# Kernel tuning notes

Measured on AMD Instinct MI355X. Metric: run time of the kernel, lower is better.

## Reference

```python
import jax, jax.numpy as jnp
import numpy as np

# --- constants from cfg (dmc.__init__) ---
DT = 3600.0            # self.t
P_SPATIAL = 21.0       # cfg.params.defaults.p
VEL_LB, VEL_UB = 0.3, 15.0
DEPTH_LB = 0.01
Q_LB = 1e-4            # discharge lower bound
BW_LB = 0.1            # bottom width lower bound
SLOPE_MIN = 1e-4
N_LO, N_HI = 0.01, 0.35          # Manning n bounds (denormalize)
QS_LO, QS_HI = 0.0, 3.0          # q_spatial bounds

# --- river network: perfect binary confluence tree, topologically ordered ---
LEVELS = 17
SIZES = [2 ** (LEVELS - 1 - l) for l in range(LEVELS)]   # 65536 leaves ... 1 outlet
OFFS = np.concatenate([[0], np.cumsum(SIZES)]).astype(np.int64)
N_NODES = int(OFFS[-1])  # 131071; internal nodes are indices OFFS[1]..N_NODES-1 (contiguous)


def _tree_edges():
    src, dst, cl, cr = [], [], [], []
    for l in range(1, LEVELS):
        k = np.arange(SIZES[l], dtype=np.int64)
        p = OFFS[l] + k
        c0 = OFFS[l - 1] + 2 * k
        c1 = OFFS[l - 1] + 2 * k + 1
        src += [c0, c1]
        dst += [p, p]
        cl.append(c0)
        cr.append(c1)
    return (np.concatenate(src).astype(np.int32), np.concatenate(dst).astype(np.int32),
            np.concatenate(cl).astype(np.int32), np.concatenate(cr).astype(np.int32))


def setup_inputs() -> dict:
    T = 336
    key = jax.random.key(0)
    ks = jax.random.split(key, 8)
    u = lambda k, s: jax.random.uniform(k, s, dtype=jnp.float32)
    q_prime = 0.1 + 5.0 * u(ks[0], (T, N_NODES))          # lateral inflow, m^3/s
    n_raw = u(ks[1], (N_NODES,))
    q_spatial_raw = u(ks[2], (N_NODES,))
    length = 500.0 + 4500.0 * u(ks[3], (N_NODES,))        # reach length, m
    slope = 1e-4 + 0.05 * u(ks[4], (N_NODES,))            # channel slope
    top_width = 2.0 + 48.0 * u(ks[5], (N_NODES,))         # m
    side_slope = 0.5 + 1.5 * u(ks[6], (N_NODES,))
    x_storage = 0.3 * u(ks[7], (N_NODES,))                # Muskingum x
    es, ed, cl, cr = _tree_edges()
    return {"q_prime": q_prime, "n_raw": n_raw, "q_spatial_raw": q_spatial_raw,
            "length": length, "slope": slope, "top_width": top_width,
            "side_slope": side_slope, "x_storage": x_storage,
            "edge_src": jnp.asarray(es), "edge_dst": jnp.asarray(ed),
            "child_left": jnp.asarray(cl), "child_right": jnp.asarray(cr)}


def _velocity(q_t, n, q_spatial, top_width, side_slope, s0):
    """_get_trapezoid_velocity: Manning's equation on a trapezoidal channel."""
    num = q_t * n * (q_spatial + 1.0)
    den = P_SPATIAL * jnp.sqrt(s0)
    depth = jnp.maximum(jnp.power(num / (den + 1e-8), 3.0 / (5.0 + 3.0 * q_spatial)), DEPTH_LB)
    bottom = jnp.maximum(top_width - 2.0 * side_slope * depth, BW_LB)
    area = (top_width + bottom) * depth * 0.5
    wetted = bottom + 2.0 * depth * jnp.sqrt(1.0 + side_slope ** 2)
    R = area / wetted
    v = (1.0 / n) * jnp.power(R, 2.0 / 3.0) * jnp.sqrt(s0)
    return jnp.clip(v, VEL_LB, VEL_UB) * (5.0 / 3.0)


def _routing(q_prime, n, qs, length, s0, top_width, side_slope, x,
             edge_src, edge_dst, child_left, child_right):
    nn = q_prime.shape[1]
    # static level scheduling for the lower-triangular solve
    parent_idx = [jnp.asarray(OFFS[l] + np.arange(SIZES[l]), dtype=jnp.int32) for l in range(1, LEVELS)]
    lvl_bounds = [(int(OFFS[l] - OFFS[1]), int(OFFS[l + 1] - OFFS[1])) for l in range(1, LEVELS)]

    def step(q, qp_prev):
        qpc = jnp.maximum(qp_prev, Q_LB)
        v = _velocity(q, n, qs, top_width, side_slope, s0)
        k = length / v
        denom = 2.0 * k * (1.0 - x) + DT
        c2 = (DT + 2.0 * k * x) / denom
        c3 = (2.0 * k * (1.0 - x) - DT) / denom
        c4 = 2.0 * DT / denom
        c1 = (DT - 2.0 * k * x) / denom
        c1_ = (-c1).at[0].set(1.0)                     # as in original (row 0 is a headwater)
        i_t = jax.ops.segment_sum(q[edge_src], edge_dst, num_segments=nn)  # N @ q
        b = c2 * i_t + c3 * q + c4 * qpc
        # solve (I + diag(c1_) N) q1 = b by forward substitution, level by level
        q1 = b                                          # leaves: q1 = b
        for li in range(LEVELS - 1):
            p = parent_idx[li]
            s, e = lvl_bounds[li]
            cl, cr = child_left[s:e], child_right[s:e]
            q1 = q1.at[p].set(b[p] - c1_[p] * (q1[cl] + q1[cr]))
        q1 = jnp.maximum(q1, Q_LB)
        return q1, q1[-1]                               # outlet gage (gage_idx = -1)

    q0 = q_prime[0]                                     # initial discharge state
    _, ys = jax.lax.scan(step, q0, q_prime[:-1])        # timesteps 1..T-1 use q_prime[t-1]
    out0 = jnp.maximum(q_prime[0, -1], Q_LB)
    return jnp.concatenate([out0[None], ys])[None, :]   # [1, T] runoff at gage


def reference(q_prime, n_raw, q_spatial_raw, length, slope, top_width, side_slope,
              x_storage, edge_src, edge_dst, child_left, child_right):
    n = N_LO + n_raw * (N_HI - N_LO)                    # denormalize
    qs = QS_LO + q_spatial_raw * (QS_HI - QS_LO)
    s0 = jnp.maximum(slope, SLOPE_MIN)
    return _routing(q_prime, n, qs, length, s0, top_width, side_slope, x_storage,
                    edge_src, edge_dst, child_left, child_right)
```

## Files before the change

### kernel.cpp

```cpp
#include <hip/hip_runtime.h>

#define Q_LBF 1e-4f
#define DTF   3600.0f
#define NN    131071
#define SENT  0x7FC00001u

#if __has_builtin(__builtin_amdgcn_exp2f)
#define FEXP2(x) __builtin_amdgcn_exp2f(x)
#else
#define FEXP2(x) exp2f(x)
#endif
#if __has_builtin(__builtin_amdgcn_logf)
#define FLOG2(x) __builtin_amdgcn_logf(x)
#else
#define FLOG2(x) log2f(x)
#endif
#if __has_builtin(__builtin_amdgcn_rcpf)
#define FRCP(x) __builtin_amdgcn_rcpf(x)
#else
#define FRCP(x) (1.0f/(x))
#endif

struct NC { float a1, e, tw, ssd, w2, a2, kd, kx; };

__device__ __forceinline__ NC make_nc(const float* __restrict__ nr,
                                      const float* __restrict__ qsr,
                                      const float* __restrict__ len,
                                      const float* __restrict__ slp,
                                      const float* __restrict__ twp,
                                      const float* __restrict__ ssp,
                                      const float* __restrict__ xsp,
                                      int g) {
  float n  = fmaf(nr[g], 0.34f, 0.01f);
  float qs = 3.0f * qsr[g];
  float s0 = fmaxf(slp[g], 1e-4f);
  float rs = sqrtf(s0);
  float L  = len[g];
  float x  = xsp[g];
  float ss = ssp[g];
  NC c;
  c.a1  = n * (qs + 1.0f) / fmaf(21.0f, rs, 1e-8f);
  c.e   = 3.0f / fmaf(3.0f, qs, 5.0f);
  c.tw  = twp[g];
  c.ssd = 2.0f * ss;
  c.w2  = 2.0f * sqrtf(fmaf(ss, ss, 1.0f));
  c.a2  = rs / n;
  float kl = 1.2f * L;
  c.kd  = kl * (1.0f - x);
  c.kx  = kl * x;
  return c;
}

__device__ __forceinline__ float node_b(const NC& c, float q, float qpc, float it,
                                        float& c1o) {
  float z    = q * c.a1;
  float d    = fmaxf(FEXP2(c.e * FLOG2(z)), 0.01f);
  float bot  = fmaxf(fmaf(-c.ssd, d, c.tw), 0.1f);
  float area = (c.tw + bot) * (0.5f * d);
  float wet  = fmaf(c.w2, d, bot);
  float R    = area * FRCP(wet);
  float v2   = c.a2 * FEXP2(0.66666668f * FLOG2(R));
  v2 = fminf(fmaxf(v2, 0.3f), 15.0f);
  float rv   = FRCP(v2);
  float rden = FRCP(fmaf(c.kd, rv, DTF));
  float c2   = fmaf(c.kx, rv, DTF) * rden;
  float c4   = 7200.0f * rden;
  c1o = c4 - c2;
  float c3 = 1.0f - c4;
  return fmaf(c2, it, fmaf(c3, q, c4 * qpc));
}

__device__ __forceinline__ int iclamp(int v, int lo, int hi) {
  return v < lo ? lo : (v > hi ? hi : v);
}

__device__ __forceinline__ void st_stream(float* p, float v) {
  __hip_atomic_store((unsigned*)p, __float_as_uint(v),
                     __ATOMIC_RELAXED, __HIP_MEMORY_SCOPE_AGENT);
}
__device__ __forceinline__ uint2 ld2_relaxed(const float* p) {
  const unsigned* u = (const unsigned*)p;
  uint2 r;
  r.x = __hip_atomic_load(u,     __ATOMIC_RELAXED, __HIP_MEMORY_SCOPE_AGENT);
  r.y = __hip_atomic_load(u + 1, __ATOMIC_RELAXED, __HIP_MEMORY_SCOPE_AGENT);
  return r;
}
__device__ __forceinline__ uint2 ld2_block(const float* p) {
  uint2 r = ld2_relaxed(p);
  while (r.x == SENT || r.y == SENT) {
    __builtin_amdgcn_s_sleep(1);
    r = ld2_relaxed(p);
  }
  return r;
}

__device__ __forceinline__ void run_A(
    const float* __restrict__ qp,
    const float* __restrict__ nr, const float* __restrict__ qsr,
    const float* __restrict__ len, const float* __restrict__ slp,
    const float* __restrict__ twp, const float* __restrict__ ssp,
    const float* __restrict__ xsp,
    float* __restrict__ S1, int wv, int lane) {
  const int g_leaf = (wv << 6) + lane;
  int e, g_int, cs0;
  if (lane < 32)      { e = 1; g_int = 65536  + (wv << 5) + lane;        cs0 = 2*lane; }
  else if (lane < 48) { e = 2; g_int = 98304  + (wv << 4) + (lane - 32); cs0 = 2*(lane-32); }
  else if (lane < 56) { e = 3; g_int = 114688 + (wv << 3) + (lane - 48); cs0 = 32 + 2*(lane-48); }
  else if (lane < 60) { e = 4; g_int = 122880 + (wv << 2) + (lane - 56); cs0 = 48 + 2*(lane-56); }
  else if (lane < 62) { e = 5; g_int = 126976 + (wv << 1) + (lane - 60); cs0 = 56 + 2*(lane-60); }
  else                { e = 6; g_int = 129024 + wv;                      cs0 = 60; }
  NC cL = make_nc(nr,qsr,len,slp,twp,ssp,xsp, g_leaf);
  NC cI = make_nc(nr,qsr,len,slp,twp,ssp,xsp, g_int);
  float q0L = qp[g_leaf];
  float q0I = qp[g_int];
  float iLa = __shfl(q0L, cs0), iLb = __shfl(q0L, cs0 + 1);
  float iIa = __shfl(q0I, cs0), iIb = __shfl(q0I, cs0 + 1);
  const bool l1 = (e == 1);
  const float itInit = l1 ? (iLa + iLb) : (iIa + iIb);
  if (lane == 62) st_stream(&S1[wv], q0I);
  float qcL = q0L, qcI = q0I, ulL = q0L, ulI = q0I;
  float pu0 = 0.0f, pu1 = 0.0f;
  float rgL[4], rgI[4];
#pragma unroll
  for (int j = 0; j < 4; ++j) {
    rgL[j] = qp[iclamp(j,     0, 335) * NN + g_leaf];
    rgI[j] = qp[iclamp(j - e, 0, 335) * NN + g_int];
  }
#pragma unroll 4
  for (int s = 0; s < 344; ++s) {
    float guL0 = __shfl(ulL, cs0), guL1 = __shfl(ulL, cs0 + 1);
    float guI0 = __shfl(ulI, cs0), guI1 = __shfl(ulI, cs0 + 1);
    float u0 = l1 ? guL0 : guI0;
    float u1 = l1 ? guL1 : guI1;
    float it = (s == e) ? itInit : (fmaxf(pu0, Q_LBF) + fmaxf(pu1, Q_LBF));
    if (s == e) qcI = q0I;
    float qpcL = fmaxf(rgL[s & 3], Q_LBF);
    float qpcI = fmaxf(rgI[s & 3], Q_LBF);
    float c1l, c1i;
    float bL = node_b(cL, qcL, qpcL, 0.0f, c1l);
    float bI = node_b(cI, qcI, qpcI, it,   c1i);
    float uIn = fmaf(c1i, u0 + u1, bI);
    qcL = fmaxf(bL,  Q_LBF); ulL = bL;
    qcI = fmaxf(uIn, Q_LBF); ulI = uIn;
    pu0 = u0; pu1 = u1;
    if (lane == 62 && s >= 6 && s <= 340) st_stream(&S1[(s - 5) * 1024 + wv], uIn);
    rgL[s & 3] = qp[iclamp(s + 4,     0, 335) * NN + g_leaf];
    rgI[s & 3] = qp[iclamp(s + 4 - e, 0, 335) * NN + g_int];
  }
}

__device__ __forceinline__ void run_B(
    const float* __restrict__ qp,
    const float* __restrict__ nr, const float* __restrict__ qsr,
    const float* __restrict__ len, const float* __restrict__ slp,
    const float* __restrict__ twp, const float* __restrict__ ssp,
    const float* __restrict__ xsp,
    const float* __restrict__ S1, float* __restrict__ S2, int r, int lane) {
  const int jl = (lane < 32) ? lane : 31;
  const int g7 = 130048 + (r << 5) + jl;
  int e, gI, cs0;
  if (lane < 16)      { e = 1; gI = 130560 + (r << 4) + lane;        cs0 = 2*lane; }
  else if (lane < 24) { e = 2; gI = 130816 + (r << 3) + (lane - 16); cs0 = 2*(lane-16); }
  else if (lane < 28) { e = 3; gI = 130944 + (r << 2) + (lane - 24); cs0 = 16 + 2*(lane-24); }
  else if (lane < 30) { e = 4; gI = 131008 + (r << 1) + (lane - 28); cs0 = 24 + 2*(lane-28); }
  else                { e = 5; gI = 131040 + r;                      cs0 = 28; }
  NC c7 = make_nc(nr,qsr,len,slp,twp,ssp,xsp, g7);
  NC cI = make_nc(nr,qsr,len,slp,twp,ssp,xsp, gI);
  float q07 = qp[g7];
  float q0I = qp[gI];
  float iLa = __shfl(q07, cs0), iLb = __shfl(q07, cs0 + 1);
  float iIa = __shfl(q0I, cs0), iIb = __shfl(q0I, cs0 + 1);
  const bool l1 = (e == 1);
  const float itInit = l1 ? (iLa + iLb) : (iIa + iIb);
  if (lane == 30) st_stream(&S2[r], q0I);
  float qc7 = q07, qcI = q0I, ul7 = q07, ulI = q0I;
  float pu0 = 0.0f, pu1 = 0.0f;
  const int col2 = ((r << 5) + jl) * 2;
  uint2 rgs[8];
  float rg7[4], rgI4[4];
#pragma unroll
  for (int j = 0; j < 8; ++j) rgs[j] = ld2_relaxed(S1 + iclamp(j, 0, 335) * 1024 + col2);
#pragma unroll
  for (int j = 0; j < 4; ++j) {
    rg7[j]  = qp[iclamp(j,     0, 335) * NN + g7];
    rgI4[j] = qp[iclamp(j - e, 0, 335) * NN + gI];
  }
#pragma unroll 8
  for (int s = 0; s < 344; ++s) {
    uint2 fo = rgs[s & 7];
    uint2 fn = rgs[(s + 1) & 7];
    if (__builtin_expect((fo.x == SENT) | (fo.y == SENT) |
                         (fn.x == SENT) | (fn.y == SENT), 0)) {
      fo = ld2_block(S1 + iclamp(s,     0, 335) * 1024 + col2);
      fn = ld2_block(S1 + iclamp(s + 1, 0, 335) * 1024 + col2);
      rgs[(s + 1) & 7] = fn;
    }
    float fox = __uint_as_float(fo.x), foy = __uint_as_float(fo.y);
    float fnx = __uint_as_float(fn.x), fny = __uint_as_float(fn.y);
    float gu0 = __shfl(ul7, cs0), gu1 = __shfl(ul7, cs0 + 1);
    float hu0 = __shfl(ulI, cs0), hu1 = __shfl(ulI, cs0 + 1);
    float u0 = l1 ? gu0 : hu0;
    float u1 = l1 ? gu1 : hu1;
    float it = (s == e) ? itInit : (fmaxf(pu0, Q_LBF) + fmaxf(pu1, Q_LBF));
    if (s == e) qcI = q0I;
    float qpc7 = fmaxf(rg7[s & 3],  Q_LBF);
    float qpcI = fmaxf(rgI4[s & 3], Q_LBF);
    float it7 = fmaxf(fox, Q_LBF) + fmaxf(foy, Q_LBF);
    float c17, c1i;
    float b7 = node_b(c7, qc7, qpc7, it7, c17);
    float u7n = fmaf(c17, fnx + fny, b7);
    float bI = node_b(cI, qcI, qpcI, it, c1i);
    float uIn = fmaf(c1i, u0 + u1, bI);
    qc7 = fmaxf(u7n, Q_LBF); ul7 = u7n;
    qcI = fmaxf(uIn, Q_LBF); ulI = uIn;
    pu0 = u0; pu1 = u1;
    if (lane == 30 && s >= 5 && s <= 339) st_stream(&S2[(s - 4) * 16 + r], uIn);
    rgs[s & 7] = ld2_relaxed(S1 + iclamp(s + 8, 0, 335) * 1024 + col2);
    rg7[s & 3]  = qp[iclamp(s + 4,     0, 335) * NN + g7];
    rgI4[s & 3] = qp[iclamp(s + 4 - e, 0, 335) * NN + gI];
  }
}

__device__ __forceinline__ void run_C(
    const float* __restrict__ qp,
    const float* __restrict__ nr, const float* __restrict__ qsr,
    const float* __restrict__ len, const float* __restrict__ slp,
    const float* __restrict__ twp, const float* __restrict__ ssp,
    const float* __restrict__ xsp,
    const float* __restrict__ S2, float* __restrict__ out, int lane) {
  const int jl = (lane < 8) ? lane : 7;
  const int g13 = 131056 + jl;
  int e, gI, cs0;
  if (lane < 4)      { e = 1; gI = 131064 + lane;       cs0 = 2*lane; }
  else if (lane < 6) { e = 2; gI = 131068 + (lane - 4); cs0 = 2*(lane-4); }
  else               { e = 3; gI = 131070;              cs0 = 4; }
  NC c13 = make_nc(nr,qsr,len,slp,twp,ssp,xsp, g13);
  NC cI  = make_nc(nr,qsr,len,slp,twp,ssp,xsp, gI);
  float q013 = qp[g13];
  float q0I  = qp[gI];
  float iLa = __shfl(q013, cs0), iLb = __shfl(q013, cs0 + 1);
  float iIa = __shfl(q0I,  cs0), iIb = __shfl(q0I,  cs0 + 1);
  const bool l1 = (e == 1);
  const float itInit = l1 ? (iLa + iLb) : (iIa + iIb);
  if (lane == 6) out[0] = fmaxf(q0I, Q_LBF);
  float qc13 = q013, qcI = q0I, ul13 = q013, ulI = q0I;
  float pu0 = 0.0f, pu1 = 0.0f;
  const int col2 = jl * 2;
  uint2 rgs[8];
  float rg13[4], rgI4[4];
#pragma unroll
  for (int j = 0; j < 8; ++j) rgs[j] = ld2_relaxed(S2 + iclamp(j, 0, 335) * 16 + col2);
#pragma unroll
  for (int j = 0; j < 4; ++j) {
    rg13[j] = qp[iclamp(j,     0, 335) * NN + g13];
    rgI4[j] = qp[iclamp(j - e, 0, 335) * NN + gI];
  }
#pragma unroll 8
  for (int s = 0; s < 344; ++s) {
    uint2 fo = rgs[s & 7];
    uint2 fn = rgs[(s + 1) & 7];
    if (__builtin_expect((fo.x == SENT) | (fo.y == SENT) |
                         (fn.x == SENT) | (fn.y == SENT), 0)) {
      fo = ld2_block(S2 + iclamp(s,     0, 335) * 16 + col2);
      fn = ld2_block(S2 + iclamp(s + 1, 0, 335) * 16 + col2);
      rgs[(s + 1) & 7] = fn;
    }
    float fox = __uint_as_float(fo.x), foy = __uint_as_float(fo.y);
    float fnx = __uint_as_float(fn.x), fny = __uint_as_float(fn.y);
    float gu0 = __shfl(ul13, cs0), gu1 = __shfl(ul13, cs0 + 1);
    float hu0 = __shfl(ulI,  cs0), hu1 = __shfl(ulI,  cs0 + 1);
    float u0 = l1 ? gu0 : hu0;
    float u1 = l1 ? gu1 : hu1;
    float it = (s == e) ? itInit : (fmaxf(pu0, Q_LBF) + fmaxf(pu1, Q_LBF));
    if (s == e) qcI = q0I;
    float qpc13 = fmaxf(rg13[s & 3], Q_LBF);
    float qpcI  = fmaxf(rgI4[s & 3], Q_LBF);
    float it13 = fmaxf(fox, Q_LBF) + fmaxf(foy, Q_LBF);
    float c113, c1i;
    float b13 = node_b(c13, qc13, qpc13, it13, c113);
    float u13n = fmaf(c113, fnx + fny, b13);
    float bI = node_b(cI, qcI, qpcI, it, c1i);
    float uIn = fmaf(c1i, u0 + u1, bI);
    qc13 = fmaxf(u13n, Q_LBF); ul13 = u13n;
    qcI  = fmaxf(uIn,  Q_LBF); ulI  = uIn;
    pu0 = u0; pu1 = u1;
    if (lane == 6 && s >= 3 && s <= 337) out[s - 2] = fmaxf(uIn, Q_LBF);
    rgs[s & 7] = ld2_relaxed(S2 + iclamp(s + 8, 0, 335) * 16 + col2);
    rg13[s & 3] = qp[iclamp(s + 4,     0, 335) * NN + g13];
    rgI4[s & 3] = qp[iclamp(s + 4 - e, 0, 335) * NN + gI];
  }
}

__global__ __launch_bounds__(256) void kinit(unsigned* __restrict__ F, int n) {
  int i = blockIdx.x * 256 + threadIdx.x;
  int stride = gridDim.x * 256;
  for (; i < n; i += stride) F[i] = SENT;
}

__global__ __launch_bounds__(320) void fused(
    const float* __restrict__ qp,
    const float* __restrict__ nr, const float* __restrict__ qsr,
    const float* __restrict__ len, const float* __restrict__ slp,
    const float* __restrict__ twp, const float* __restrict__ ssp,
    const float* __restrict__ xsp,
    float* __restrict__ S1, float* __restrict__ S2,
    float* __restrict__ out) {
  const int wave = threadIdx.x >> 6;
  const int lane = threadIdx.x & 63;
  if (wave < 4) {
    run_A(qp, nr, qsr, len, slp, twp, ssp, xsp, S1,
          (blockIdx.x << 2) + wave, lane);
  } else if (blockIdx.x < 16) {
    run_B(qp, nr, qsr, len, slp, twp, ssp, xsp, S1, S2, blockIdx.x, lane);
  } else if (blockIdx.x == 16) {
    run_C(qp, nr, qsr, len, slp, twp, ssp, xsp, S2, out, lane);
  }
}

extern "C" void kernel_launch(void* const* d_in, const int* in_sizes, int n_in,
                              void* d_out, int out_size, void* d_ws, size_t ws_size,
                              hipStream_t stream) {
  const float* q_prime = (const float*)d_in[0];
  const float* n_raw   = (const float*)d_in[1];
  const float* qs_raw  = (const float*)d_in[2];
  const float* length  = (const float*)d_in[3];
  const float* slope   = (const float*)d_in[4];
  const float* tw      = (const float*)d_in[5];
  const float* ss      = (const float*)d_in[6];
  const float* xs      = (const float*)d_in[7];
  float* out = (float*)d_out;
  float* S1 = (float*)d_ws;
  float* S2 = S1 + 337 * 1024;
  const int nsent = 337 * 1024 + 337 * 16;
  kinit<<<128, 256, 0, stream>>>((unsigned*)d_ws, nsent);
  fused<<<256, 320, 0, stream>>>(q_prime, n_raw, qs_raw, length, slope, tw, ss, xs,
                                 S1, S2, out);
}
```

Before: 372.1 us.

## Repartition tree levels so each lane handles one node per step

Each wave now maps one node per lane: 32 leaves plus a 5-level internal subtree. Previously each lane computed both a leaf and an internal node, and half the internal-node work was masked. The change doubles the number of stage-A waves (2048, in 512-thread blocks), shifts stage B and C level boundaries to match, widens the handoff buffers, and routes predicated stores to dummy slots. Prefetch depth grows to 8 with pointer-increment addressing in place of per-iteration clamps. This halves the serial per-step node_b work per lane at the cost of more waves and a deeper stage-B/C chain.

```diff
diff --git a/kernel.cpp b/kernel.cpp
--- a/kernel.cpp
+++ b/kernel.cpp
@@ -4,6 +4,8 @@
 #define DTF   3600.0f
 #define NN    131071
 #define SENT  0x7FC00001u
+#define W1    2048
+#define W2    32
 
 #if __has_builtin(__builtin_amdgcn_exp2f)
 #define FEXP2(x) __builtin_amdgcn_exp2f(x)
@@ -100,52 +102,43 @@
     const float* __restrict__ len, const float* __restrict__ slp,
     const float* __restrict__ twp, const float* __restrict__ ssp,
     const float* __restrict__ xsp,
-    float* __restrict__ S1, int wv, int lane) {
-  const int g_leaf = (wv << 6) + lane;
-  int e, g_int, cs0;
-  if (lane < 32)      { e = 1; g_int = 65536  + (wv << 5) + lane;        cs0 = 2*lane; }
-  else if (lane < 48) { e = 2; g_int = 98304  + (wv << 4) + (lane - 32); cs0 = 2*(lane-32); }
-  else if (lane < 56) { e = 3; g_int = 114688 + (wv << 3) + (lane - 48); cs0 = 32 + 2*(lane-48); }
-  else if (lane < 60) { e = 4; g_int = 122880 + (wv << 2) + (lane - 56); cs0 = 48 + 2*(lane-56); }
-  else if (lane < 62) { e = 5; g_int = 126976 + (wv << 1) + (lane - 60); cs0 = 56 + 2*(lane-60); }
-  else                { e = 6; g_int = 129024 + wv;                      cs0 = 60; }
-  NC cL = make_nc(nr,qsr,len,slp,twp,ssp,xsp, g_leaf);
-  NC cI = make_nc(nr,qsr,len,slp,twp,ssp,xsp, g_int);
-  float q0L = qp[g_leaf];
-  float q0I = qp[g_int];
-  float iLa = __shfl(q0L, cs0), iLb = __shfl(q0L, cs0 + 1);
-  float iIa = __shfl(q0I, cs0), iIb = __shfl(q0I, cs0 + 1);
-  const bool l1 = (e == 1);
-  const float itInit = l1 ? (iLa + iLb) : (iIa + iIb);
-  if (lane == 62) st_stream(&S1[wv], q0I);
-  float qcL = q0L, qcI = q0I, ulL = q0L, ulI = q0I;
-  float pu0 = 0.0f, pu1 = 0.0f;
-  float rgL[4], rgI[4];
-#pragma unroll
-  for (int j = 0; j < 4; ++j) {
-    rgL[j] = qp[iclamp(j,     0, 335) * NN + g_leaf];
-    rgI[j] = qp[iclamp(j - e, 0, 335) * NN + g_int];
-  }
-#pragma unroll 4
+    float* __restrict__ S1, float* __restrict__ D1, int w, int lane) {
+  int e, g, cs0;
+  const bool leaf = lane < 32;
+  if (leaf)           { e = 0; g = (w << 5) + lane;               cs0 = 0; }
+  else if (lane < 48) { e = 1; g = 65536  + (w << 4) + (lane-32); cs0 = 2*(lane-32); }
+  else if (lane < 56) { e = 2; g = 98304  + (w << 3) + (lane-48); cs0 = 32 + 2*(lane-48); }
+  else if (lane < 60) { e = 3; g = 114688 + (w << 2) + (lane-56); cs0 = 48 + 2*(lane-56); }
+  else if (lane < 62) { e = 4; g = 122880 + (w << 1) + (lane-60); cs0 = 56 + 2*(lane-60); }
+  else                { e = 5; g = 126976 + w;                    cs0 = 60; }
+  NC c = make_nc(nr,qsr,len,slp,twp,ssp,xsp, g);
+  float q0 = qp[g];
+  float i0 = __shfl(q0, cs0), i1 = __shfl(q0, cs0 + 1);
+  const float itInit = i0 + i1;
+  if (lane == 62) st_stream(&S1[w], q0);
+  float qc = q0, ul = q0, pu0 = 0.0f, pu1 = 0.0f;
+  float rg[8];
+#pragma unroll
+  for (int j = 0; j < 8; ++j) rg[j] = qp[iclamp(j - e, 0, 335) * NN + g];
+  int off = (8 - e) * NN + g;
+  const int offMax = 335 * NN + g;
+#pragma unroll 8
   for (int s = 0; s < 344; ++s) {
-    float guL0 = __shfl(ulL, cs0), guL1 = __shfl(ulL, cs0 + 1);
-    float guI0 = __shfl(ulI, cs0), guI1 = __shfl(ulI, cs0 + 1);
-    float u0 = l1 ? guL0 : guI0;
-    float u1 = l1 ? guL1 : guI1;
-    float it = (s == e) ? itInit : (fmaxf(pu0, Q_LBF) + fmaxf(pu1, Q_LBF));
-    if (s == e) qcI = q0I;
-    float qpcL = fmaxf(rgL[s & 3], Q_LBF);
-    float qpcI = fmaxf(rgI[s & 3], Q_LBF);
-    float c1l, c1i;
-    float bL = node_b(cL, qcL, qpcL, 0.0f, c1l);
-    float bI = node_b(cI, qcI, qpcI, it,   c1i);
-    float uIn = fmaf(c1i, u0 + u1, bI);
-    qcL = fmaxf(bL,  Q_LBF); ulL = bL;
-    qcI = fmaxf(uIn, Q_LBF); ulI = uIn;
+    float u0 = __shfl(ul, cs0), u1 = __shfl(ul, cs0 + 1);
+    float itg = (s == e) ? itInit : (fmaxf(pu0, Q_LBF) + fmaxf(pu1, Q_LBF));
+    if (s == e) qc = q0;
+    float it  = leaf ? 0.0f : itg;
+    float chn = leaf ? 0.0f : (u0 + u1);
+    float qpc = fmaxf(rg[s & 7], Q_LBF);
+    float c1;
+    float b  = node_b(c, qc, qpc, it, c1);
+    float un = fmaf(c1, chn, b);
+    qc = fmaxf(un, Q_LBF); ul = un;
     pu0 = u0; pu1 = u1;
-    if (lane == 62 && s >= 6 && s <= 340) st_stream(&S1[(s - 5) * 1024 + wv], uIn);
-    rgL[s & 3] = qp[iclamp(s + 4,     0, 335) * NN + g_leaf];
-    rgI[s & 3] = qp[iclamp(s + 4 - e, 0, 335) * NN + g_int];
+    float* dst = (s >= 5 && s <= 339) ? (S1 + (s - 4) * W1 + w) : (D1 + w);
+    if (lane == 62) st_stream(dst, un);
+    rg[s & 7] = qp[off];
+    off = min(off + NN, offMax);
   }
 }
 
@@ -155,69 +148,63 @@
     const float* __restrict__ len, const float* __restrict__ slp,
     const float* __restrict__ twp, const float* __restrict__ ssp,
     const float* __restrict__ xsp,
-    const float* __restrict__ S1, float* __restrict__ S2, int r, int lane) {
-  const int jl = (lane < 32) ? lane : 31;
-  const int g7 = 130048 + (r << 5) + jl;
-  int e, gI, cs0;
-  if (lane < 16)      { e = 1; gI = 130560 + (r << 4) + lane;        cs0 = 2*lane; }
-  else if (lane < 24) { e = 2; gI = 130816 + (r << 3) + (lane - 16); cs0 = 2*(lane-16); }
-  else if (lane < 28) { e = 3; gI = 130944 + (r << 2) + (lane - 24); cs0 = 16 + 2*(lane-24); }
-  else if (lane < 30) { e = 4; gI = 131008 + (r << 1) + (lane - 28); cs0 = 24 + 2*(lane-28); }
-  else                { e = 5; gI = 131040 + r;                      cs0 = 28; }
-  NC c7 = make_nc(nr,qsr,len,slp,twp,ssp,xsp, g7);
-  NC cI = make_nc(nr,qsr,len,slp,twp,ssp,xsp, gI);
-  float q07 = qp[g7];
-  float q0I = qp[gI];
-  float iLa = __shfl(q07, cs0), iLb = __shfl(q07, cs0 + 1);
-  float iIa = __shfl(q0I, cs0), iIb = __shfl(q0I, cs0 + 1);
-  const bool l1 = (e == 1);
-  const float itInit = l1 ? (iLa + iLb) : (iIa + iIb);
-  if (lane == 30) st_stream(&S2[r], q0I);
-  float qc7 = q07, qcI = q0I, ul7 = q07, ulI = q0I;
-  float pu0 = 0.0f, pu1 = 0.0f;
+    const float* __restrict__ S1, float* __restrict__ S2,
+    float* __restrict__ D2, int r, int lane) {
+  int e, g, cs0;
+  const bool leaf = lane < 32;
+  const int jl = leaf ? lane : 31;
+  if (leaf)           { e = 0; g = 129024 + (r << 5) + lane;      cs0 = 0; }
+  else if (lane < 48) { e = 1; g = 130048 + (r << 4) + (lane-32); cs0 = 2*(lane-32); }
+  else if (lane < 56) { e = 2; g = 130560 + (r << 3) + (lane-48); cs0 = 32 + 2*(lane-48); }
+  else if (lane < 60) { e = 3; g = 130816 + (r << 2) + (lane-56); cs0 = 48 + 2*(lane-56); }
+  else if (lane < 62) { e = 4; g = 130944 + (r << 1) + (lane-60); cs0 = 56 + 2*(lane-60); }
+  else                { e = 5; g = 131008 + r;                    cs0 = 60; }
   const int col2 = ((r << 5) + jl) * 2;
+  NC c = make_nc(nr,qsr,len,slp,twp,ssp,xsp, g);
+  float q0 = qp[g];
+  float i0 = __shfl(q0, cs0), i1 = __shfl(q0, cs0 + 1);
+  const float itInit = i0 + i1;
+  if (lane == 62) st_stream(&S2[r], q0);
+  float qc = q0, ul = q0, pu0 = 0.0f, pu1 = 0.0f;
   uint2 rgs[8];
-  float rg7[4], rgI4[4];
-#pragma unroll
-  for (int j = 0; j < 8; ++j) rgs[j] = ld2_relaxed(S1 + iclamp(j, 0, 335) * 1024 + col2);
-#pragma unroll
-  for (int j = 0; j < 4; ++j) {
-    rg7[j]  = qp[iclamp(j,     0, 335) * NN + g7];
-    rgI4[j] = qp[iclamp(j - e, 0, 335) * NN + gI];
-  }
+  float rg[8];
+#pragma unroll
+  for (int j = 0; j < 8; ++j) rgs[j] = ld2_relaxed(S1 + iclamp(j, 0, 335) * W1 + col2);
+#pragma unroll
+  for (int j = 0; j < 8; ++j) rg[j] = qp[iclamp(j - e, 0, 335) * NN + g];
+  int off = (8 - e) * NN + g;
+  const int offMax = 335 * NN + g;
+  int soff = 8 * W1 + col2;
+  const int soffMax = 335 * W1 + col2;
 #pragma unroll 8
   for (int s = 0; s < 344; ++s) {
     uint2 fo = rgs[s & 7];
     uint2 fn = rgs[(s + 1) & 7];
     if (__builtin_expect((fo.x == SENT) | (fo.y == SENT) |
                          (fn.x == SENT) | (fn.y == SENT), 0)) {
-      fo = ld2_block(S1 + iclamp(s,     0, 335) * 1024 + col2);
-      fn = ld2_block(S1 + iclamp(s + 1, 0, 335) * 1024 + col2);
+      fo = ld2_block(S1 + iclamp(s,     0, 335) * W1 + col2);
+      fn = ld2_block(S1 + iclamp(s + 1, 0, 335) * W1 + col2);
       rgs[(s + 1) & 7] = fn;
     }
     float fox = __uint_as_float(fo.x), foy = __uint_as_float(fo.y);
     float fnx = __uint_as_float(fn.x), fny = __uint_as_float(fn.y);
-    float gu0 = __shfl(ul7, cs0), gu1 = __shfl(ul7, cs0 + 1);
-    float hu0 = __shfl(ulI, cs0), hu1 = __shfl(ulI, cs0 + 1);
-    float u0 = l1 ? gu0 : hu0;
-    float u1 = l1 ? gu1 : hu1;
-    float it = (s == e) ? itInit : (fmaxf(pu0, Q_LBF) + fmaxf(pu1, Q_LBF));
-    if (s == e) qcI = q0I;
-    float qpc7 = fmaxf(rg7[s & 3],  Q_LBF);
-    float qpcI = fmaxf(rgI4[s & 3], Q_LBF);
-    float it7 = fmaxf(fox, Q_LBF) + fmaxf(foy, Q_LBF);
-    float c17, c1i;
-    float b7 = node_b(c7, qc7, qpc7, it7, c17);
-    float u7n = fmaf(c17, fnx + fny, b7);
-    float bI = node_b(cI, qcI, qpcI, it, c1i);
-    float uIn = fmaf(c1i, u0 + u1, bI);
-    qc7 = fmaxf(u7n, Q_LBF); ul7 = u7n;
-    qcI = fmaxf(uIn, Q_LBF); ulI = uIn;
+    float u0 = __shfl(ul, cs0), u1 = __shfl(ul, cs0 + 1);
+    float itg = (s == e) ? itInit : (fmaxf(pu0, Q_LBF) + fmaxf(pu1, Q_LBF));
+    if (s == e) qc = q0;
+    float it  = leaf ? (fmaxf(fox, Q_LBF) + fmaxf(foy, Q_LBF)) : itg;
+    float chn = leaf ? (fnx + fny) : (u0 + u1);
+    float qpc = fmaxf(rg[s & 7], Q_LBF);
+    float c1;
+    float b  = node_b(c, qc, qpc, it, c1);
+    float un = fmaf(c1, chn, b);
+    qc = fmaxf(un, Q_LBF); ul = un;
     pu0 = u0; pu1 = u1;
-    if (lane == 30 && s >= 5 && s <= 339) st_stream(&S2[(s - 4) * 16 + r], uIn);
-    rgs[s & 7] = ld2_relaxed(S1 + iclamp(s + 8, 0, 335) * 1024 + col2);
-    rg7[s & 3]  = qp[iclamp(s + 4,     0, 335) * NN + g7];
-    rgI4[s & 3] = qp[iclamp(s + 4 - e, 0, 335) * NN + gI];
+    float* dst = (s >= 5 && s <= 339) ? (S2 + (s - 4) * W2 + r) : (D2 + r);
+    if (lane == 62) st_stream(dst, un);
+    rgs[s & 7] = ld2_relaxed(S1 + soff);
+    rg[s & 7]  = qp[off];
+    off  = min(off + NN, offMax);
+    soff = min(soff + W1, soffMax);
   }
 }
 
@@ -228,66 +215,59 @@
     const float* __restrict__ twp, const float* __restrict__ ssp,
     const float* __restrict__ xsp,
     const float* __restrict__ S2, float* __restrict__ out, int lane) {
-  const int jl = (lane < 8) ? lane : 7;
-  const int g13 = 131056 + jl;
-  int e, gI, cs0;
-  if (lane < 4)      { e = 1; gI = 131064 + lane;       cs0 = 2*lane; }
-  else if (lane < 6) { e = 2; gI = 131068 + (lane - 4); cs0 = 2*(lane-4); }
-  else               { e = 3; gI = 131070;              cs0 = 4; }
-  NC c13 = make_nc(nr,qsr,len,slp,twp,ssp,xsp, g13);
-  NC cI  = make_nc(nr,qsr,len,slp,twp,ssp,xsp, gI);
-  float q013 = qp[g13];
-  float q0I  = qp[gI];
-  float iLa = __shfl(q013, cs0), iLb = __shfl(q013, cs0 + 1);
-  float iIa = __shfl(q0I,  cs0), iIb = __shfl(q0I,  cs0 + 1);
-  const bool l1 = (e == 1);
-  const float itInit = l1 ? (iLa + iLb) : (iIa + iIb);
-  if (lane == 6) out[0] = fmaxf(q0I, Q_LBF);
-  float qc13 = q013, qcI = q0I, ul13 = q013, ulI = q0I;
-  float pu0 = 0.0f, pu1 = 0.0f;
+  int e, g, cs0;
+  const bool leaf = lane < 16;
+  const int jl = leaf ? lane : 15;
+  if (leaf)           { e = 0; g = 131040 + lane;        cs0 = 0; }
+  else if (lane < 24) { e = 1; g = 131056 + (lane - 16); cs0 = 2*(lane-16); }
+  else if (lane < 28) { e = 2; g = 131064 + (lane - 24); cs0 = 16 + 2*(lane-24); }
+  else if (lane < 30) { e = 3; g = 131068 + (lane - 28); cs0 = 24 + 2*(lane-28); }
+  else                { e = 4; g = 131070;               cs0 = 28; }
   const int col2 = jl * 2;
+  NC c = make_nc(nr,qsr,len,slp,twp,ssp,xsp, g);
+  float q0 = qp[g];
+  float i0 = __shfl(q0, cs0), i1 = __shfl(q0, cs0 + 1);
+  const float itInit = i0 + i1;
+  if (lane == 30) out[0] = fmaxf(q0, Q_LBF);
+  float qc = q0, ul = q0, pu0 = 0.0f, pu1 = 0.0f;
   uint2 rgs[8];
-  float rg13[4], rgI4[4];
-#pragma unroll
-  for (int j = 0; j < 8; ++j) rgs[j] = ld2_relaxed(S2 + iclamp(j, 0, 335) * 16 + col2);
-#pragma unroll
-  for (int j = 0; j < 4; ++j) {
-    rg13[j] = qp[iclamp(j,     0, 335) * NN + g13];
-    rgI4[j] = qp[iclamp(j - e, 0, 335) * NN + gI];
-  }
+  float rg[8];
+#pragma unroll
+  for (int j = 0; j < 8; ++j) rgs[j] = ld2_relaxed(S2 + iclamp(j, 0, 335) * W2 + col2);
+#pragma unroll
+  for (int j = 0; j < 8; ++j) rg[j] = qp[iclamp(j - e, 0, 335) * NN + g];
+  int off = (8 - e) * NN + g;
+  const int offMax = 335 * NN + g;
+  int soff = 8 * W2 + col2;
+  const int soffMax = 335 * W2 + col2;
 #pragma unroll 8
   for (int s = 0; s < 344; ++s) {
     uint2 fo = rgs[s & 7];
     uint2 fn = rgs[(s + 1) & 7];
     if (__builtin_expect((fo.x == SENT) | (fo.y == SENT) |
                          (fn.x == SENT) | (fn.y == SENT), 0)) {
-      fo = ld2_block(S2 + iclamp(s,     0, 335) * 16 + col2);
-      fn = ld2_block(S2 + iclamp(s + 1, 0, 335) * 16 + col2);
+      fo = ld2_block(S2 + iclamp(s,     0, 335) * W2 + col2);
+      fn = ld2_block(S2 + iclamp(s + 1, 0, 335) * W2 + col2);
       rgs[(s + 1) & 7] = fn;
     }
     float fox = __uint_as_float(fo.x), foy = __uint_as_float(fo.y);
     float fnx = __uint_as_float(fn.x), fny = __uint_as_float(fn.y);
-    float gu0 = __shfl(ul13, cs0), gu1 = __shfl(ul13, cs0 + 1);
-    float hu0 = __shfl(ulI,  cs0), hu1 = __shfl(ulI,  cs0 + 1);
-    float u0 = l1 ? gu0 : hu0;
-    float u1 = l1 ? gu1 : hu1;
-    float it = (s == e) ? itInit : (fmaxf(pu0, Q_LBF) + fmaxf(pu1, Q_LBF));
-    if (s == e) qcI = q0I;
-    float qpc13 = fmaxf(rg13[s & 3], Q_LBF);
-    float qpcI  = fmaxf(rgI4[s & 3], Q_LBF);
-    float it13 = fmaxf(fox, Q_LBF) + fmaxf(foy, Q_LBF);
-    float c113, c1i;
-    float b13 = node_b(c13, qc13, qpc13, it13, c113);
-    float u13n = fmaf(c113, fnx + fny, b13);
-    float bI = node_b(cI, qcI, qpcI, it, c1i);
-    float uIn = fmaf(c1i, u0 + u1, bI);
-    qc13 = fmaxf(u13n, Q_LBF); ul13 = u13n;
-    qcI  = fmaxf(uIn,  Q_LBF); ulI  = uIn;
+    float u0 = __shfl(ul, cs0), u1 = __shfl(ul, cs0 + 1);
+    float itg = (s == e) ? itInit : (fmaxf(pu0, Q_LBF) + fmaxf(pu1, Q_LBF));
+    if (s == e) qc = q0;
+    float it  = leaf ? (fmaxf(fox, Q_LBF) + fmaxf(foy, Q_LBF)) : itg;
+    float chn = leaf ? (fnx + fny) : (u0 + u1);
+    float qpc = fmaxf(rg[s & 7], Q_LBF);
+    float c1;
+    float b  = node_b(c, qc, qpc, it, c1);
+    float un = fmaf(c1, chn, b);
+    qc = fmaxf(un, Q_LBF); ul = un;
     pu0 = u0; pu1 = u1;
-    if (lane == 6 && s >= 3 && s <= 337) out[s - 2] = fmaxf(uIn, Q_LBF);
-    rgs[s & 7] = ld2_relaxed(S2 + iclamp(s + 8, 0, 335) * 16 + col2);
-    rg13[s & 3] = qp[iclamp(s + 4,     0, 335) * NN + g13];
-    rgI4[s & 3] = qp[iclamp(s + 4 - e, 0, 335) * NN + gI];
+    if (lane == 30 && s >= 4 && s <= 338) out[s - 3] = fmaxf(un, Q_LBF);
+    rgs[s & 7] = ld2_relaxed(S2 + soff);
+    rg[s & 7]  = qp[off];
+    off  = min(off + NN, offMax);
+    soff = min(soff + W2, soffMax);
   }
 }
 
@@ -297,22 +277,24 @@
   for (; i < n; i += stride) F[i] = SENT;
 }
 
-__global__ __launch_bounds__(320) void fused(
+__global__ __launch_bounds__(512) void fused(
     const float* __restrict__ qp,
     const float* __restrict__ nr, const float* __restrict__ qsr,
     const float* __restrict__ len, const float* __restrict__ slp,
     const float* __restrict__ twp, const float* __restrict__ ssp,
     const float* __restrict__ xsp,
     float* __restrict__ S1, float* __restrict__ S2,
+    float* __restrict__ D1, float* __restrict__ D2,
     float* __restrict__ out) {
-  const int wave = threadIdx.x >> 6;
+  const int wv = threadIdx.x >> 6;
   const int lane = threadIdx.x & 63;
-  if (wave < 4) {
-    run_A(qp, nr, qsr, len, slp, twp, ssp, xsp, S1,
-          (blockIdx.x << 2) + wave, lane);
-  } else if (blockIdx.x < 16) {
-    run_B(qp, nr, qsr, len, slp, twp, ssp, xsp, S1, S2, blockIdx.x, lane);
-  } else if (blockIdx.x == 16) {
+  const int b = blockIdx.x;
+  if (b < 256) {
+    run_A(qp, nr, qsr, len, slp, twp, ssp, xsp, S1, D1, (b << 3) + wv, lane);
+  } else if (b < 260) {
+    run_B(qp, nr, qsr, len, slp, twp, ssp, xsp, S1, S2, D2,
+          ((b - 256) << 3) + wv, lane);
+  } else if (wv == 0) {
     run_C(qp, nr, qsr, len, slp, twp, ssp, xsp, S2, out, lane);
   }
 }
@@ -330,9 +312,11 @@
   const float* xs      = (const float*)d_in[7];
   float* out = (float*)d_out;
   float* S1 = (float*)d_ws;
-  float* S2 = S1 + 337 * 1024;
-  const int nsent = 337 * 1024 + 337 * 16;
+  float* S2 = S1 + 336 * W1;
+  float* D1 = S2 + 336 * W2;
+  float* D2 = D1 + W1;
+  const int nsent = 336 * W1 + 336 * W2 + W1 + W2;
   kinit<<<128, 256, 0, stream>>>((unsigned*)d_ws, nsent);
-  fused<<<256, 320, 0, stream>>>(q_prime, n_raw, qs_raw, length, slope, tw, ss, xs,
-                                 S1, S2, out);
-}
+  fused<<<261, 512, 0, stream>>>(q_prime, n_raw, qs_raw, length, slope, tw, ss, xs,
+                                 S1, S2, D1, D2, out);
+}
```

New measurement: 376.8 us. Within noise of the previous version (+1.3%).
